# Performance work log

Measured on AMD Instinct MI355X. Metric: run time of the kernel, lower is better.

Reference implementation:

```python
import jax, jax.numpy as jnp
import numpy as np

L, B, S, D, H, FF = 6, 4, 1024, 256, 8, 128
DH = D // H
EPS = 1e-5


def _ln(x, w, b):
    m = x.mean(-1, keepdims=True)
    v = ((x - m) ** 2).mean(-1, keepdims=True)
    return (x - m) / jnp.sqrt(v + EPS) * w + b


def setup_inputs() -> dict:
    key = jax.random.key(0)
    ks = jax.random.split(key, 6)
    s = lambda k, shape: jax.random.normal(k, shape, jnp.float32) * 0.02
    return {
        "x": jax.random.normal(ks[0], (B, S, D), jnp.float32),
        "ln1_w": jnp.ones((L, D), jnp.float32),
        "ln1_b": jnp.zeros((L, D), jnp.float32),
        "wqkv": s(ks[1], (L, D, 3 * D)),   # qkv_linear, bias=False
        "wout": s(ks[2], (L, D, D)),       # out_linear, bias=False
        "ln2_w": jnp.ones((L, D), jnp.float32),
        "ln2_b": jnp.zeros((L, D), jnp.float32),
        "w1": s(ks[3], (L, D, 2 * FF)),    # Linear(d_model, 2*ff)
        "b1": jnp.zeros((L, 2 * FF), jnp.float32),
        "w2": s(ks[4], (L, FF, D)),        # Linear(ff, d_model)
        "b2": jnp.zeros((L, D), jnp.float32),
    }


def reference(x, ln1_w, ln1_b, wqkv, wout, ln2_w, ln2_b, w1, b1, w2, b2):
    attn_weights_list = []
    scale = 1.0 / jnp.sqrt(jnp.float32(DH))
    for i in range(L):
        # --- pre-norm multi-head attention ---
        xn = _ln(x, ln1_w[i], ln1_b[i])
        qkv = xn @ wqkv[i]                       # [B,S,3D]
        q, k, v = jnp.split(qkv, 3, axis=-1)
        rs = lambda t: t.reshape(B, S, H, DH).transpose(0, 2, 1, 3)  # b h s d
        q, k, v = rs(q), rs(k), rs(v)
        logits = jnp.einsum('bhid,bhjd->bhij', q, k) * scale
        aw = jax.nn.softmax(logits, axis=-1)     # [B,H,S,S] (dropout=0, eval)
        attn_weights_list.append(aw)
        o = jnp.einsum('bhij,bhjd->bhid', aw, v)
        o = o.transpose(0, 2, 1, 3).reshape(B, S, D) @ wout[i]
        x = x + o
        # --- pre-norm GEGLU FFN ---
        h = _ln(x, ln2_w[i], ln2_b[i]) @ w1[i] + b1[i]   # [B,S,2*FF]
        a, g = jnp.split(h, 2, axis=-1)
        x = x + (a * jax.nn.gelu(g, approximate=False)) @ w2[i] + b2[i]
    return x, jnp.stack(attn_weights_list)      # [B,S,D], [L,B,H,S,S]
```

## Files before the change

### kernel.cpp

```cpp
#include <hip/hip_runtime.h>
#include <hip/hip_bf16.h>

typedef __bf16 bf16x8 __attribute__((ext_vector_type(8)));
typedef __bf16 bf16x4 __attribute__((ext_vector_type(4)));
typedef float  f32x4  __attribute__((ext_vector_type(4)));

#define LAYERS 6
#define BATCH  4
#define SEQ    1024
#define DMODEL 256
#define NHEAD  8
#define DHEAD  32
#define FFDIM  128
#define ROWS   (BATCH*SEQ)
#define QKVN   (3*DMODEL)
#define QSCALE 0.2550348616f

static __device__ __forceinline__ bf16x8 ldg8(const __bf16* p) {
  return *reinterpret_cast<const bf16x8*>(p);
}
#define MFMA16(a, b, c) __builtin_amdgcn_mfma_f32_16x16x32_bf16((a), (b), (c), 0, 0, 0)

__global__ __launch_bounds__(256) void k_prepT(const float* __restrict__ in,
                                               __bf16* __restrict__ out,
                                               int R, int C) {
  __shared__ __bf16 T[64][72];
  int l = blockIdx.z, r0 = blockIdx.y * 64, c0 = blockIdx.x * 64;
  const float* src = in + ((size_t)l * R + r0) * C + c0;
  int tr = threadIdx.x >> 6, tc = threadIdx.x & 63;
  #pragma unroll 4
  for (int it = 0; it < 16; ++it) {
    int r = it * 4 + tr;
    T[r][tc] = (__bf16)src[(size_t)r * C + tc];
  }
  __syncthreads();
  __bf16* dst = out + ((size_t)l * C + c0) * R + r0;
  #pragma unroll 4
  for (int it = 0; it < 16; ++it) {
    int c = it * 4 + tr;
    dst[(size_t)c * R + tc] = T[tc][c];
  }
}

__global__ __launch_bounds__(64) void k_ln(const float* __restrict__ x,
                                           const float* __restrict__ w,
                                           const float* __restrict__ b,
                                           __bf16* __restrict__ out) {
  int row = blockIdx.x, l = threadIdx.x;
  const float* xr = x + (size_t)row * DMODEL;
  float v[4];
  #pragma unroll
  for (int j = 0; j < 4; ++j) v[j] = xr[l + 64 * j];
  float s = v[0] + v[1] + v[2] + v[3];
  #pragma unroll
  for (int off = 32; off >= 1; off >>= 1) s += __shfl_xor(s, off);
  float mean = s * (1.0f / DMODEL);
  float sq = 0.f;
  #pragma unroll
  for (int j = 0; j < 4; ++j) { v[j] -= mean; sq += v[j] * v[j]; }
  #pragma unroll
  for (int off = 32; off >= 1; off >>= 1) sq += __shfl_xor(sq, off);
  float rstd = rsqrtf(sq * (1.0f / DMODEL) + 1e-5f);
  __bf16* orow = out + (size_t)row * DMODEL;
  #pragma unroll
  for (int j = 0; j < 4; ++j) {
    int c = l + 64 * j;
    orow[c] = (__bf16)(v[j] * rstd * w[c] + b[c]);
  }
}

__global__ __launch_bounds__(256) void k_qkv(const __bf16* __restrict__ xn,
                                             const __bf16* __restrict__ Bt,
                                             __bf16* __restrict__ qb,
                                             __bf16* __restrict__ kt,
                                             __bf16* __restrict__ vt) {
  int w = threadIdx.x >> 6, l = threadIdx.x & 63, lr = l & 15, lg = l >> 4;
  int m0 = blockIdx.x * 64 + w * 16;
  int n0 = blockIdx.y * 64;
  f32x4 acc[4] = {};
  const __bf16* ap = xn + (size_t)(m0 + lr) * DMODEL + 8 * lg;
  const __bf16* bp = Bt + (size_t)(n0 + lr) * DMODEL + 8 * lg;
  for (int kc = 0; kc < DMODEL; kc += 32) {
    bf16x8 a = ldg8(ap + kc);
    #pragma unroll
    for (int t = 0; t < 4; ++t) {
      bf16x8 b = ldg8(bp + (size_t)t * 16 * DMODEL + kc);
      acc[t] = MFMA16(a, b, acc[t]);
    }
  }
  int row = m0 + lg * 4;
  if (n0 < DMODEL) {
    #pragma unroll
    for (int t = 0; t < 4; ++t) {
      int col = n0 + t * 16 + lr;
      #pragma unroll
      for (int r = 0; r < 4; ++r)
        qb[(size_t)(row + r) * DMODEL + col] = (__bf16)(acc[t][r] * QSCALE);
    }
  } else if (n0 < 2 * DMODEL) {
    int b_ = row >> 10, s = row & (SEQ - 1);
    #pragma unroll
    for (int t = 0; t < 4; ++t) {
      int hdh = n0 - DMODEL + t * 16 + lr;
      int h = hdh >> 5, dh = hdh & 31;
      size_t base = ((size_t)(b_ * NHEAD + h) * SEQ + s) * DHEAD + dh;
      #pragma unroll
      for (int r = 0; r < 4; ++r) kt[base + (size_t)r * DHEAD] = (__bf16)acc[t][r];
    }
  } else {
    int b_ = row >> 10, s = row & (SEQ - 1);
    #pragma unroll
    for (int t = 0; t < 4; ++t) {
      int hdh = n0 - 2 * DMODEL + t * 16 + lr;
      int h = hdh >> 5, dh = hdh & 31;
      bf16x4 v4;
      #pragma unroll
      for (int r = 0; r < 4; ++r) v4[r] = (__bf16)acc[t][r];
      *reinterpret_cast<bf16x4*>(vt + ((size_t)(b_ * NHEAD + h) * DHEAD + dh) * SEQ + s) = v4;
    }
  }
}

__global__ __launch_bounds__(512, 6) void k_attn(const __bf16* __restrict__ qb,
                                                 const __bf16* __restrict__ kt,
                                                 const __bf16* __restrict__ vt,
                                                 __bf16* __restrict__ ob,
                                                 float* __restrict__ aw) {
  __shared__ __bf16 P[8][2][16][40];
  __shared__ float  Ssum[8][16];
  __shared__ float  OS[8][16][34];
  int bid = blockIdx.x;
  int swz = (bid & 7) * 256 + (bid >> 3);
  int qblk = swz & 63, h = (swz >> 6) & 7, b = swz >> 9;
  int w = threadIdx.x >> 6, l = threadIdx.x & 63, lr = l & 15, lg = l >> 4;
  int q0 = qblk * 16;
  bf16x8 qf = ldg8(qb + ((size_t)(b * SEQ) + q0 + lr) * DMODEL + h * DHEAD + 8 * lg);
  const __bf16* ktb = kt + (size_t)(b * NHEAD + h) * SEQ * DHEAD + 8 * lg;
  const __bf16* vtb = vt + (size_t)(b * NHEAD + h) * DHEAD * SEQ;
  f32x4 z = {};
  int kbeg = w * 128;

  float s4[4] = {0.f, 0.f, 0.f, 0.f};
  #pragma unroll 4
  for (int t = 0; t < 8; ++t) {
    bf16x8 kf = ldg8(ktb + (size_t)(kbeg + t * 16 + lr) * DHEAD);
    f32x4 d = MFMA16(qf, kf, z);
    #pragma unroll
    for (int r = 0; r < 4; ++r) s4[r] += exp2f(d[r]);
  }
  #pragma unroll
  for (int off = 1; off < 16; off <<= 1) {
    #pragma unroll
    for (int r = 0; r < 4; ++r) s4[r] += __shfl_xor(s4[r], off);
  }
  if (lr == 0) {
    #pragma unroll
    for (int r = 0; r < 4; ++r) Ssum[w][lg * 4 + r] = s4[r];
  }
  __syncthreads();
  float rinv[4];
  #pragma unroll
  for (int r = 0; r < 4; ++r) {
    int row = lg * 4 + r;
    float s = Ssum[0][row] + Ssum[1][row] + Ssum[2][row] + Ssum[3][row]
            + Ssum[4][row] + Ssum[5][row] + Ssum[6][row] + Ssum[7][row];
    rinv[r] = 1.0f / s;
  }

  float* awb = aw + ((size_t)(b * NHEAD + h) * SEQ) * SEQ;
  float (*ST)[32] = reinterpret_cast<float(*)[32]>(&OS[w][0][0]);

#define QK_TILE(KC, BUF)                                                          \
  {                                                                               \
    _Pragma("unroll")                                                             \
    for (int half = 0; half < 2; ++half) {                                        \
      int k0 = (KC) + half * 16;                                                  \
      bf16x8 kf = ldg8(ktb + (size_t)(k0 + lr) * DHEAD);                          \
      f32x4 d = MFMA16(qf, kf, z);                                                \
      _Pragma("unroll")                                                           \
      for (int r = 0; r < 4; ++r) {                                               \
        float pn = exp2f(d[r]) * rinv[r];                                         \
        ST[lg * 4 + r][half * 16 + lr] = pn;                                      \
        P[w][BUF][lg * 4 + r][half * 16 + lr] = (__bf16)pn;                       \
      }                                                                           \
    }                                                                             \
  }

#define FLUSH(KC)                                                                 \
  {                                                                               \
    int frow = l >> 3, fcol = (l & 7) * 4;                                        \
    f32x4 v0 = *reinterpret_cast<const f32x4*>(&ST[frow][fcol]);                  \
    f32x4 v1 = *reinterpret_cast<const f32x4*>(&ST[frow + 8][fcol]);              \
    *reinterpret_cast<f32x4*>(&awb[(size_t)(q0 + frow) * SEQ + (KC) + fcol]) = v0;\
    *reinterpret_cast<f32x4*>(&awb[(size_t)(q0 + frow + 8) * SEQ + (KC) + fcol]) = v1;\
  }

  f32x4 accO[2] = {};
  QK_TILE(kbeg, 0)
  #pragma unroll
  for (int j = 1; j < 4; ++j) {
    int kc = kbeg + j * 32;
    bf16x8 pf  = *reinterpret_cast<const bf16x8*>(&P[w][(j - 1) & 1][lr][8 * lg]);
    bf16x8 vf0 = ldg8(vtb + (size_t)lr * SEQ + (kc - 32) + 8 * lg);
    bf16x8 vf1 = ldg8(vtb + (size_t)(16 + lr) * SEQ + (kc - 32) + 8 * lg);
    FLUSH(kc - 32)
    QK_TILE(kc, j & 1)
    accO[0] = MFMA16(pf, vf0, accO[0]);
    accO[1] = MFMA16(pf, vf1, accO[1]);
  }
  {
    bf16x8 pf  = *reinterpret_cast<const bf16x8*>(&P[w][1][lr][8 * lg]);
    bf16x8 vf0 = ldg8(vtb + (size_t)lr * SEQ + (kbeg + 96) + 8 * lg);
    bf16x8 vf1 = ldg8(vtb + (size_t)(16 + lr) * SEQ + (kbeg + 96) + 8 * lg);
    FLUSH(kbeg + 96)
    accO[0] = MFMA16(pf, vf0, accO[0]);
    accO[1] = MFMA16(pf, vf1, accO[1]);
  }
#undef QK_TILE
#undef FLUSH

  #pragma unroll
  for (int t = 0; t < 2; ++t)
    #pragma unroll
    for (int r = 0; r < 4; ++r) OS[w][lg * 4 + r][t * 16 + lr] = accO[t][r];
  __syncthreads();
  int row = threadIdx.x >> 5, col = threadIdx.x & 31;
  float o = 0.f;
  #pragma unroll
  for (int ww = 0; ww < 8; ++ww) o += OS[ww][row][col];
  ob[((size_t)(b * SEQ) + q0 + row) * DMODEL + h * DHEAD + col] = (__bf16)o;
}

template <int LAST>
__global__ __launch_bounds__(512) void k_pf(const __bf16* __restrict__ ob,
                                            const __bf16* __restrict__ woutT,
                                            const float* __restrict__ xres,
                                            const float* __restrict__ ln2w,
                                            const float* __restrict__ ln2b,
                                            const __bf16* __restrict__ w1t,
                                            const float* __restrict__ b1,
                                            const __bf16* __restrict__ w2t,
                                            const float* __restrict__ b2,
                                            float* __restrict__ x32out,
                                            const float* __restrict__ lnw_n,
                                            const float* __restrict__ lnb_n,
                                            const __bf16* __restrict__ wqkvT_n,
                                            __bf16* __restrict__ qb,
                                            __bf16* __restrict__ kt,
                                            __bf16* __restrict__ vt,
                                            float* __restrict__ xout) {
  __shared__ float  xs[16][268];
  __shared__ __bf16 XN[16][264];
  __shared__ __bf16 HT[16][136];
  int w = threadIdx.x >> 6, l = threadIdx.x & 63, lr = l & 15, lg = l >> 4;
  int m0 = blockIdx.x * 16;
  {
    int n0 = w * 32;
    f32x4 acc[2] = {};
    const __bf16* ap = ob + (size_t)(m0 + lr) * DMODEL + 8 * lg;
    const __bf16* bp = woutT + (size_t)(n0 + lr) * DMODEL + 8 * lg;
    for (int kc = 0; kc < DMODEL; kc += 32) {
      bf16x8 a = ldg8(ap + kc);
      #pragma unroll
      for (int t = 0; t < 2; ++t)
        acc[t] = MFMA16(a, ldg8(bp + (size_t)t * 16 * DMODEL + kc), acc[t]);
    }
    #pragma unroll
    for (int t = 0; t < 2; ++t) {
      int col = n0 + t * 16 + lr;
      #pragma unroll
      for (int r = 0; r < 4; ++r) {
        int row = lg * 4 + r;
        xs[row][col] = acc[t][r] + xres[(size_t)(m0 + row) * DMODEL + col];
      }
    }
  }
  __syncthreads();
  #pragma unroll
  for (int rr = 0; rr < 2; ++rr) {
    int row = w * 2 + rr;
    f32x4 v = *reinterpret_cast<const f32x4*>(&xs[row][4 * l]);
    float s = v[0] + v[1] + v[2] + v[3];
    #pragma unroll
    for (int off = 32; off >= 1; off >>= 1) s += __shfl_xor(s, off);
    float mean = s * (1.0f / DMODEL);
    float sq = 0.f;
    f32x4 c;
    #pragma unroll
    for (int j = 0; j < 4; ++j) { c[j] = v[j] - mean; sq += c[j] * c[j]; }
    #pragma unroll
    for (int off = 32; off >= 1; off >>= 1) sq += __shfl_xor(sq, off);
    float rstd = rsqrtf(sq * (1.0f / DMODEL) + 1e-5f);
    f32x4 lwv = *reinterpret_cast<const f32x4*>(&ln2w[4 * l]);
    f32x4 lbv = *reinterpret_cast<const f32x4*>(&ln2b[4 * l]);
    bf16x4 o4;
    #pragma unroll
    for (int j = 0; j < 4; ++j) o4[j] = (__bf16)(c[j] * rstd * lwv[j] + lbv[j]);
    *reinterpret_cast<bf16x4*>(&XN[row][4 * l]) = o4;
  }
  __syncthreads();
  {
    f32x4 acc1[2] = {};
    const __bf16* bpa = w1t + (size_t)(w * 16 + lr) * DMODEL + 8 * lg;
    const __bf16* bpg = w1t + (size_t)(128 + w * 16 + lr) * DMODEL + 8 * lg;
    for (int kc = 0; kc < DMODEL; kc += 32) {
      bf16x8 a = *reinterpret_cast<const bf16x8*>(&XN[lr][kc + 8 * lg]);
      acc1[0] = MFMA16(a, ldg8(bpa + kc), acc1[0]);
      acc1[1] = MFMA16(a, ldg8(bpg + kc), acc1[1]);
    }
    int fc = w * 16 + lr;
    #pragma unroll
    for (int r = 0; r < 4; ++r) {
      float a1 = acc1[0][r] + b1[fc];
      float g  = acc1[1][r] + b1[fc + 128];
      float ge = 0.5f * g * (1.0f + erff(g * 0.70710678118654752f));
      HT[lg * 4 + r][fc] = (__bf16)(a1 * ge);
    }
  }
  __syncthreads();
  {
    int n0 = w * 32;
    f32x4 acc2[2] = {};
    const __bf16* bp = w2t + (size_t)(n0 + lr) * FFDIM + 8 * lg;
    for (int kc = 0; kc < FFDIM; kc += 32) {
      bf16x8 a2 = *reinterpret_cast<const bf16x8*>(&HT[lr][kc + 8 * lg]);
      #pragma unroll
      for (int t = 0; t < 2; ++t)
        acc2[t] = MFMA16(a2, ldg8(bp + (size_t)t * 16 * FFDIM + kc), acc2[t]);
    }
    #pragma unroll
    for (int t = 0; t < 2; ++t) {
      int col = n0 + t * 16 + lr;
      #pragma unroll
      for (int r = 0; r < 4; ++r) {
        int row = lg * 4 + r;
        xs[row][col] = acc2[t][r] + b2[col] + xs[row][col];
      }
    }
  }
  __syncthreads();
  #pragma unroll
  for (int rr = 0; rr < 2; ++rr) {
    int row = w * 2 + rr;
    f32x4 v = *reinterpret_cast<const f32x4*>(&xs[row][4 * l]);
    if (LAST) {
      *reinterpret_cast<f32x4*>(&xout[(size_t)(m0 + row) * DMODEL + 4 * l]) = v;
    } else {
      float s = v[0] + v[1] + v[2] + v[3];
      #pragma unroll
      for (int off = 32; off >= 1; off >>= 1) s += __shfl_xor(s, off);
      float mean = s * (1.0f / DMODEL);
      float sq = 0.f;
      f32x4 c;
      #pragma unroll
      for (int j = 0; j < 4; ++j) { c[j] = v[j] - mean; sq += c[j] * c[j]; }
      #pragma unroll
      for (int off = 32; off >= 1; off >>= 1) sq += __shfl_xor(sq, off);
      float rstd = rsqrtf(sq * (1.0f / DMODEL) + 1e-5f);
      *reinterpret_cast<f32x4*>(&x32out[(size_t)(m0 + row) * DMODEL + 4 * l]) = v;
      f32x4 lwv = *reinterpret_cast<const f32x4*>(&lnw_n[4 * l]);
      f32x4 lbv = *reinterpret_cast<const f32x4*>(&lnb_n[4 * l]);
      bf16x4 o4;
      #pragma unroll
      for (int j = 0; j < 4; ++j) o4[j] = (__bf16)(c[j] * rstd * lwv[j] + lbv[j]);
      *reinterpret_cast<bf16x4*>(&XN[row][4 * l]) = o4;
    }
  }
  if (!LAST) {
    __syncthreads();
    f32x4 acc[6] = {};
    {
      const __bf16* bp = wqkvT_n + (size_t)(w * 96 + lr) * DMODEL + 8 * lg;
      for (int kc = 0; kc < DMODEL; kc += 32) {
        bf16x8 a = *reinterpret_cast<const bf16x8*>(&XN[lr][kc + 8 * lg]);
        #pragma unroll
        for (int t = 0; t < 6; ++t)
          acc[t] = MFMA16(a, ldg8(bp + (size_t)t * 16 * DMODEL + kc), acc[t]);
      }
    }
    int row = m0 + lg * 4;
    int b_ = row >> 10, s = row & (SEQ - 1);
    #pragma unroll
    for (int t = 0; t < 6; ++t) {
      int col = w * 96 + t * 16 + lr;
      if (col < DMODEL) {
        #pragma unroll
        for (int r = 0; r < 4; ++r)
          qb[(size_t)(row + r) * DMODEL + col] = (__bf16)(acc[t][r] * QSCALE);
      } else if (col < 2 * DMODEL) {
        int hdh = col - DMODEL;
        int h = hdh >> 5, dh = hdh & 31;
        size_t base = ((size_t)(b_ * NHEAD + h) * SEQ + s) * DHEAD + dh;
        #pragma unroll
        for (int r = 0; r < 4; ++r) kt[base + (size_t)r * DHEAD] = (__bf16)acc[t][r];
      } else {
        int hdh = col - 2 * DMODEL;
        int h = hdh >> 5, dh = hdh & 31;
        bf16x4 v4;
        #pragma unroll
        for (int r = 0; r < 4; ++r) v4[r] = (__bf16)acc[t][r];
        *reinterpret_cast<bf16x4*>(vt + ((size_t)(b_ * NHEAD + h) * DHEAD + dh) * SEQ + s) = v4;
      }
    }
  }
}

static inline size_t align256(size_t x) { return (x + 255) & ~(size_t)255; }

extern "C" void kernel_launch(void* const* d_in, const int* in_sizes, int n_in,
                              void* d_out, int out_size, void* d_ws, size_t ws_size,
                              hipStream_t stream) {
  const float* x_in = (const float*)d_in[0];
  const float* ln1w = (const float*)d_in[1];
  const float* ln1b = (const float*)d_in[2];
  const float* wqkv = (const float*)d_in[3];
  const float* wout = (const float*)d_in[4];
  const float* ln2w = (const float*)d_in[5];
  const float* ln2b = (const float*)d_in[6];
  const float* w1   = (const float*)d_in[7];
  const float* b1   = (const float*)d_in[8];
  const float* w2   = (const float*)d_in[9];
  const float* b2   = (const float*)d_in[10];
  float* out = (float*)d_out;

  char* p = (char*)d_ws;
  float*  x32   = (float*)p;  p += align256((size_t)ROWS * DMODEL * 4);
  __bf16* xn    = (__bf16*)p; p += align256((size_t)ROWS * DMODEL * 2);
  __bf16* qb    = (__bf16*)p; p += align256((size_t)ROWS * DMODEL * 2);
  __bf16* kt    = (__bf16*)p; p += align256((size_t)ROWS * DMODEL * 2);
  __bf16* vt    = (__bf16*)p; p += align256((size_t)ROWS * DMODEL * 2);
  __bf16* ob    = (__bf16*)p; p += align256((size_t)ROWS * DMODEL * 2);
  __bf16* wqkvT = (__bf16*)p; p += align256((size_t)LAYERS * DMODEL * QKVN * 2);
  __bf16* woutT = (__bf16*)p; p += align256((size_t)LAYERS * DMODEL * DMODEL * 2);
  __bf16* w1T   = (__bf16*)p; p += align256((size_t)LAYERS * DMODEL * 2 * FFDIM * 2);
  __bf16* w2T   = (__bf16*)p; p += align256((size_t)LAYERS * FFDIM * DMODEL * 2);

  k_prepT<<<dim3(QKVN / 64, DMODEL / 64, LAYERS), 256, 0, stream>>>(wqkv, wqkvT, DMODEL, QKVN);
  k_prepT<<<dim3(DMODEL / 64, DMODEL / 64, LAYERS), 256, 0, stream>>>(wout, woutT, DMODEL, DMODEL);
  k_prepT<<<dim3(2 * FFDIM / 64, DMODEL / 64, LAYERS), 256, 0, stream>>>(w1, w1T, DMODEL, 2 * FFDIM);
  k_prepT<<<dim3(DMODEL / 64, FFDIM / 64, LAYERS), 256, 0, stream>>>(w2, w2T, FFDIM, DMODEL);
  k_ln<<<ROWS, 64, 0, stream>>>(x_in, ln1w, ln1b, xn);
  k_qkv<<<dim3(ROWS / 64, QKVN / 64), 256, 0, stream>>>(xn, wqkvT, qb, kt, vt);

  const size_t AW_LAYER = (size_t)BATCH * NHEAD * SEQ * SEQ;
  for (int i = 0; i < LAYERS; ++i) {
    float* aw_l = out + (size_t)ROWS * DMODEL + (size_t)i * AW_LAYER;
    k_attn<<<SEQ / 16 * NHEAD * BATCH, 512, 0, stream>>>(qb, kt, vt, ob, aw_l);
    const float* xres = (i == 0) ? x_in : x32;
    if (i < LAYERS - 1) {
      k_pf<0><<<ROWS / 16, 512, 0, stream>>>(
          ob, woutT + (size_t)i * DMODEL * DMODEL, xres,
          ln2w + i * DMODEL, ln2b + i * DMODEL,
          w1T + (size_t)i * DMODEL * 2 * FFDIM, b1 + i * 2 * FFDIM,
          w2T + (size_t)i * FFDIM * DMODEL, b2 + i * DMODEL,
          x32, ln1w + (i + 1) * DMODEL, ln1b + (i + 1) * DMODEL,
          wqkvT + (size_t)(i + 1) * DMODEL * QKVN, qb, kt, vt, nullptr);
    } else {
      k_pf<1><<<ROWS / 16, 512, 0, stream>>>(
          ob, woutT + (size_t)i * DMODEL * DMODEL, xres,
          ln2w + i * DMODEL, ln2b + i * DMODEL,
          w1T + (size_t)i * DMODEL * 2 * FFDIM, b1 + i * 2 * FFDIM,
          w2T + (size_t)i * FFDIM * DMODEL, b2 + i * DMODEL,
          x32, nullptr, nullptr, nullptr, nullptr, nullptr, nullptr, out);
    }
  }
}
```

Measured before the change: 444.7 us.

## Move attention-weight writes into fused post-attention kernel with double-buffered QKV

The attention kernel now does a single pass: it accumulates unnormalized softmax sums alongside the PV product, normalizes the output at the end, and stores per-row reciprocal sums. The big fp32 attention-weight writes move into extra blocks of the fused out-proj/FFN/next-QKV kernel, which recompute QK^T, scale by the stored reciprocals, and write with nontemporal stores. QKV buffers are double-buffered so the next layer's projections do not overwrite data those blocks still read. This removes the separate sum pre-pass and overlaps the memory-bound weight stores with FFN compute, at the cost of recomputing the QK^T product and extra workspace.

New measurement: 460.5 us. +3.6%, slower.

```diff
diff --git a/kernel.cpp b/kernel.cpp
--- a/kernel.cpp
+++ b/kernel.cpp
@@ -15,6 +15,8 @@
 #define ROWS   (BATCH*SEQ)
 #define QKVN   (3*DMODEL)
 #define QSCALE 0.2550348616f
+#define PFBLKS (ROWS/16)
+#define AWBLKS (SEQ/16*NHEAD*BATCH)
 
 static __device__ __forceinline__ bf16x8 ldg8(const __bf16* p) {
   return *reinterpret_cast<const bf16x8*>(p);
@@ -125,7 +127,7 @@
                                                  const __bf16* __restrict__ kt,
                                                  const __bf16* __restrict__ vt,
                                                  __bf16* __restrict__ ob,
-                                                 float* __restrict__ aw) {
+                                                 float* __restrict__ rb) {
   __shared__ __bf16 P[8][2][16][40];
   __shared__ float  Ssum[8][16];
   __shared__ float  OS[8][16][34];
@@ -141,34 +143,6 @@
   int kbeg = w * 128;
 
   float s4[4] = {0.f, 0.f, 0.f, 0.f};
-  #pragma unroll 4
-  for (int t = 0; t < 8; ++t) {
-    bf16x8 kf = ldg8(ktb + (size_t)(kbeg + t * 16 + lr) * DHEAD);
-    f32x4 d = MFMA16(qf, kf, z);
-    #pragma unroll
-    for (int r = 0; r < 4; ++r) s4[r] += exp2f(d[r]);
-  }
-  #pragma unroll
-  for (int off = 1; off < 16; off <<= 1) {
-    #pragma unroll
-    for (int r = 0; r < 4; ++r) s4[r] += __shfl_xor(s4[r], off);
-  }
-  if (lr == 0) {
-    #pragma unroll
-    for (int r = 0; r < 4; ++r) Ssum[w][lg * 4 + r] = s4[r];
-  }
-  __syncthreads();
-  float rinv[4];
-  #pragma unroll
-  for (int r = 0; r < 4; ++r) {
-    int row = lg * 4 + r;
-    float s = Ssum[0][row] + Ssum[1][row] + Ssum[2][row] + Ssum[3][row]
-            + Ssum[4][row] + Ssum[5][row] + Ssum[6][row] + Ssum[7][row];
-    rinv[r] = 1.0f / s;
-  }
-
-  float* awb = aw + ((size_t)(b * NHEAD + h) * SEQ) * SEQ;
-  float (*ST)[32] = reinterpret_cast<float(*)[32]>(&OS[w][0][0]);
 
 #define QK_TILE(KC, BUF)                                                          \
   {                                                                               \
@@ -179,20 +153,11 @@
       f32x4 d = MFMA16(qf, kf, z);                                                \
       _Pragma("unroll")                                                           \
       for (int r = 0; r < 4; ++r) {                                               \
-        float pn = exp2f(d[r]) * rinv[r];                                         \
-        ST[lg * 4 + r][half * 16 + lr] = pn;                                      \
-        P[w][BUF][lg * 4 + r][half * 16 + lr] = (__bf16)pn;                       \
+        float pv = exp2f(d[r]);                                                   \
+        s4[r] += pv;                                                              \
+        P[w][BUF][lg * 4 + r][half * 16 + lr] = (__bf16)pv;                       \
       }                                                                           \
     }                                                                             \
-  }
-
-#define FLUSH(KC)                                                                 \
-  {                                                                               \
-    int frow = l >> 3, fcol = (l & 7) * 4;                                        \
-    f32x4 v0 = *reinterpret_cast<const f32x4*>(&ST[frow][fcol]);                  \
-    f32x4 v1 = *reinterpret_cast<const f32x4*>(&ST[frow + 8][fcol]);              \
-    *reinterpret_cast<f32x4*>(&awb[(size_t)(q0 + frow) * SEQ + (KC) + fcol]) = v0;\
-    *reinterpret_cast<f32x4*>(&awb[(size_t)(q0 + frow + 8) * SEQ + (KC) + fcol]) = v1;\
   }
 
   f32x4 accO[2] = {};
@@ -203,7 +168,6 @@
     bf16x8 pf  = *reinterpret_cast<const bf16x8*>(&P[w][(j - 1) & 1][lr][8 * lg]);
     bf16x8 vf0 = ldg8(vtb + (size_t)lr * SEQ + (kc - 32) + 8 * lg);
     bf16x8 vf1 = ldg8(vtb + (size_t)(16 + lr) * SEQ + (kc - 32) + 8 * lg);
-    FLUSH(kc - 32)
     QK_TILE(kc, j & 1)
     accO[0] = MFMA16(pf, vf0, accO[0]);
     accO[1] = MFMA16(pf, vf1, accO[1]);
@@ -212,17 +176,40 @@
     bf16x8 pf  = *reinterpret_cast<const bf16x8*>(&P[w][1][lr][8 * lg]);
     bf16x8 vf0 = ldg8(vtb + (size_t)lr * SEQ + (kbeg + 96) + 8 * lg);
     bf16x8 vf1 = ldg8(vtb + (size_t)(16 + lr) * SEQ + (kbeg + 96) + 8 * lg);
-    FLUSH(kbeg + 96)
     accO[0] = MFMA16(pf, vf0, accO[0]);
     accO[1] = MFMA16(pf, vf1, accO[1]);
   }
 #undef QK_TILE
-#undef FLUSH
+
+  #pragma unroll
+  for (int off = 1; off < 16; off <<= 1) {
+    #pragma unroll
+    for (int r = 0; r < 4; ++r) s4[r] += __shfl_xor(s4[r], off);
+  }
+  if (lr == 0) {
+    #pragma unroll
+    for (int r = 0; r < 4; ++r) Ssum[w][lg * 4 + r] = s4[r];
+  }
+  __syncthreads();
+  float rinv[4];
+  #pragma unroll
+  for (int r = 0; r < 4; ++r) {
+    int row = lg * 4 + r;
+    float s = Ssum[0][row] + Ssum[1][row] + Ssum[2][row] + Ssum[3][row]
+            + Ssum[4][row] + Ssum[5][row] + Ssum[6][row] + Ssum[7][row];
+    rinv[r] = 1.0f / s;
+  }
+  if (w == 0 && l < 16) {
+    float s = 0.f;
+    #pragma unroll
+    for (int ww = 0; ww < 8; ++ww) s += Ssum[ww][l];
+    rb[((size_t)(b * SEQ) + q0 + l) * NHEAD + h] = 1.0f / s;
+  }
 
   #pragma unroll
   for (int t = 0; t < 2; ++t)
     #pragma unroll
-    for (int r = 0; r < 4; ++r) OS[w][lg * 4 + r][t * 16 + lr] = accO[t][r];
+    for (int r = 0; r < 4; ++r) OS[w][lg * 4 + r][t * 16 + lr] = accO[t][r] * rinv[r];
   __syncthreads();
   int row = threadIdx.x >> 5, col = threadIdx.x & 31;
   float o = 0.f;
@@ -232,27 +219,69 @@
 }
 
 template <int LAST>
-__global__ __launch_bounds__(512) void k_pf(const __bf16* __restrict__ ob,
-                                            const __bf16* __restrict__ woutT,
-                                            const float* __restrict__ xres,
-                                            const float* __restrict__ ln2w,
-                                            const float* __restrict__ ln2b,
-                                            const __bf16* __restrict__ w1t,
-                                            const float* __restrict__ b1,
-                                            const __bf16* __restrict__ w2t,
-                                            const float* __restrict__ b2,
-                                            float* __restrict__ x32out,
-                                            const float* __restrict__ lnw_n,
-                                            const float* __restrict__ lnb_n,
-                                            const __bf16* __restrict__ wqkvT_n,
-                                            __bf16* __restrict__ qb,
-                                            __bf16* __restrict__ kt,
-                                            __bf16* __restrict__ vt,
-                                            float* __restrict__ xout) {
-  __shared__ float  xs[16][268];
-  __shared__ __bf16 XN[16][264];
-  __shared__ __bf16 HT[16][136];
+__global__ __launch_bounds__(512) void k_pfaw(const __bf16* __restrict__ ob,
+                                              const __bf16* __restrict__ qbr,
+                                              const __bf16* __restrict__ ktr,
+                                              const float* __restrict__ rb,
+                                              float* __restrict__ aw,
+                                              const __bf16* __restrict__ woutT,
+                                              const float* __restrict__ xres,
+                                              const float* __restrict__ ln2w,
+                                              const float* __restrict__ ln2b,
+                                              const __bf16* __restrict__ w1t,
+                                              const float* __restrict__ b1,
+                                              const __bf16* __restrict__ w2t,
+                                              const float* __restrict__ b2,
+                                              float* __restrict__ x32out,
+                                              const float* __restrict__ lnw_n,
+                                              const float* __restrict__ lnb_n,
+                                              const __bf16* __restrict__ wqkvT_n,
+                                              __bf16* __restrict__ qb_n,
+                                              __bf16* __restrict__ kt_n,
+                                              __bf16* __restrict__ vt_n,
+                                              float* __restrict__ xout) {
+  __shared__ char smem[17152 + 8448 + 4352];
   int w = threadIdx.x >> 6, l = threadIdx.x & 63, lr = l & 15, lg = l >> 4;
+
+  if (blockIdx.x >= PFBLKS) {
+    float (*ST)[16][32] = reinterpret_cast<float(*)[16][32]>(smem);
+    int bid = blockIdx.x - PFBLKS;
+    int swz = (bid & 7) * 256 + (bid >> 3);
+    int qblk = swz & 63, h = (swz >> 6) & 7, b = swz >> 9;
+    int q0 = qblk * 16;
+    bf16x8 qf = ldg8(qbr + ((size_t)(b * SEQ) + q0 + lr) * DMODEL + h * DHEAD + 8 * lg);
+    const __bf16* ktb = ktr + (size_t)(b * NHEAD + h) * SEQ * DHEAD + 8 * lg;
+    float rv[4];
+    #pragma unroll
+    for (int r = 0; r < 4; ++r)
+      rv[r] = rb[((size_t)(b * SEQ) + q0 + lg * 4 + r) * NHEAD + h];
+    float* awb = aw + ((size_t)(b * NHEAD + h) * SEQ) * SEQ;
+    f32x4 z = {};
+    int kbeg = w * 128;
+    #pragma unroll
+    for (int t0 = 0; t0 < 8; ++t0) {
+      bf16x8 kf = ldg8(ktb + (size_t)(kbeg + t0 * 16 + lr) * DHEAD);
+      f32x4 d = MFMA16(qf, kf, z);
+      #pragma unroll
+      for (int r = 0; r < 4; ++r)
+        ST[w][lg * 4 + r][(t0 & 1) * 16 + lr] = exp2f(d[r]) * rv[r];
+      if (t0 & 1) {
+        int frow = l >> 3, fcol = (l & 7) * 4;
+        int kc = kbeg + (t0 - 1) * 16;
+        f32x4 v0 = *reinterpret_cast<const f32x4*>(&ST[w][frow][fcol]);
+        f32x4 v1 = *reinterpret_cast<const f32x4*>(&ST[w][frow + 8][fcol]);
+        __builtin_nontemporal_store(v0, reinterpret_cast<f32x4*>(
+            &awb[(size_t)(q0 + frow) * SEQ + kc + fcol]));
+        __builtin_nontemporal_store(v1, reinterpret_cast<f32x4*>(
+            &awb[(size_t)(q0 + frow + 8) * SEQ + kc + fcol]));
+      }
+    }
+    return;
+  }
+
+  float  (*xs)[268] = reinterpret_cast<float(*)[268]>(smem);
+  __bf16 (*XN)[264] = reinterpret_cast<__bf16(*)[264]>(smem + 17152);
+  __bf16 (*HT)[136] = reinterpret_cast<__bf16(*)[136]>(smem + 17152 + 8448);
   int m0 = blockIdx.x * 16;
   {
     int n0 = w * 32;
@@ -386,20 +415,20 @@
       if (col < DMODEL) {
         #pragma unroll
         for (int r = 0; r < 4; ++r)
-          qb[(size_t)(row + r) * DMODEL + col] = (__bf16)(acc[t][r] * QSCALE);
+          qb_n[(size_t)(row + r) * DMODEL + col] = (__bf16)(acc[t][r] * QSCALE);
       } else if (col < 2 * DMODEL) {
         int hdh = col - DMODEL;
         int h = hdh >> 5, dh = hdh & 31;
         size_t base = ((size_t)(b_ * NHEAD + h) * SEQ + s) * DHEAD + dh;
         #pragma unroll
-        for (int r = 0; r < 4; ++r) kt[base + (size_t)r * DHEAD] = (__bf16)acc[t][r];
+        for (int r = 0; r < 4; ++r) kt_n[base + (size_t)r * DHEAD] = (__bf16)acc[t][r];
       } else {
         int hdh = col - 2 * DMODEL;
         int h = hdh >> 5, dh = hdh & 31;
         bf16x4 v4;
         #pragma unroll
         for (int r = 0; r < 4; ++r) v4[r] = (__bf16)acc[t][r];
-        *reinterpret_cast<bf16x4*>(vt + ((size_t)(b_ * NHEAD + h) * DHEAD + dh) * SEQ + s) = v4;
+        *reinterpret_cast<bf16x4*>(vt_n + ((size_t)(b_ * NHEAD + h) * DHEAD + dh) * SEQ + s) = v4;
       }
     }
   }
@@ -426,10 +455,14 @@
   char* p = (char*)d_ws;
   float*  x32   = (float*)p;  p += align256((size_t)ROWS * DMODEL * 4);
   __bf16* xn    = (__bf16*)p; p += align256((size_t)ROWS * DMODEL * 2);
-  __bf16* qb    = (__bf16*)p; p += align256((size_t)ROWS * DMODEL * 2);
-  __bf16* kt    = (__bf16*)p; p += align256((size_t)ROWS * DMODEL * 2);
-  __bf16* vt    = (__bf16*)p; p += align256((size_t)ROWS * DMODEL * 2);
+  __bf16* qbA   = (__bf16*)p; p += align256((size_t)ROWS * DMODEL * 2);
+  __bf16* ktA   = (__bf16*)p; p += align256((size_t)ROWS * DMODEL * 2);
+  __bf16* vtA   = (__bf16*)p; p += align256((size_t)ROWS * DMODEL * 2);
+  __bf16* qbB   = (__bf16*)p; p += align256((size_t)ROWS * DMODEL * 2);
+  __bf16* ktB   = (__bf16*)p; p += align256((size_t)ROWS * DMODEL * 2);
+  __bf16* vtB   = (__bf16*)p; p += align256((size_t)ROWS * DMODEL * 2);
   __bf16* ob    = (__bf16*)p; p += align256((size_t)ROWS * DMODEL * 2);
+  float*  rb    = (float*)p;  p += align256((size_t)ROWS * NHEAD * 4);
   __bf16* wqkvT = (__bf16*)p; p += align256((size_t)LAYERS * DMODEL * QKVN * 2);
   __bf16* woutT = (__bf16*)p; p += align256((size_t)LAYERS * DMODEL * DMODEL * 2);
   __bf16* w1T   = (__bf16*)p; p += align256((size_t)LAYERS * DMODEL * 2 * FFDIM * 2);
@@ -440,24 +473,32 @@
   k_prepT<<<dim3(2 * FFDIM / 64, DMODEL / 64, LAYERS), 256, 0, stream>>>(w1, w1T, DMODEL, 2 * FFDIM);
   k_prepT<<<dim3(DMODEL / 64, FFDIM / 64, LAYERS), 256, 0, stream>>>(w2, w2T, FFDIM, DMODEL);
   k_ln<<<ROWS, 64, 0, stream>>>(x_in, ln1w, ln1b, xn);
-  k_qkv<<<dim3(ROWS / 64, QKVN / 64), 256, 0, stream>>>(xn, wqkvT, qb, kt, vt);
+  k_qkv<<<dim3(ROWS / 64, QKVN / 64), 256, 0, stream>>>(xn, wqkvT, qbA, ktA, vtA);
 
   const size_t AW_LAYER = (size_t)BATCH * NHEAD * SEQ * SEQ;
   for (int i = 0; i < LAYERS; ++i) {
     float* aw_l = out + (size_t)ROWS * DMODEL + (size_t)i * AW_LAYER;
-    k_attn<<<SEQ / 16 * NHEAD * BATCH, 512, 0, stream>>>(qb, kt, vt, ob, aw_l);
     const float* xres = (i == 0) ? x_in : x32;
+    __bf16* qb_c = (i & 1) ? qbB : qbA;
+    __bf16* kt_c = (i & 1) ? ktB : ktA;
+    __bf16* vt_c = (i & 1) ? vtB : vtA;
+    __bf16* qb_n = (i & 1) ? qbA : qbB;
+    __bf16* kt_n = (i & 1) ? ktA : ktB;
+    __bf16* vt_n = (i & 1) ? vtA : vtB;
+    k_attn<<<AWBLKS, 512, 0, stream>>>(qb_c, kt_c, vt_c, ob, rb);
     if (i < LAYERS - 1) {
-      k_pf<0><<<ROWS / 16, 512, 0, stream>>>(
-          ob, woutT + (size_t)i * DMODEL * DMODEL, xres,
+      k_pfaw<0><<<PFBLKS + AWBLKS, 512, 0, stream>>>(
+          ob, qb_c, kt_c, rb, aw_l,
+          woutT + (size_t)i * DMODEL * DMODEL, xres,
           ln2w + i * DMODEL, ln2b + i * DMODEL,
           w1T + (size_t)i * DMODEL * 2 * FFDIM, b1 + i * 2 * FFDIM,
           w2T + (size_t)i * FFDIM * DMODEL, b2 + i * DMODEL,
           x32, ln1w + (i + 1) * DMODEL, ln1b + (i + 1) * DMODEL,
-          wqkvT + (size_t)(i + 1) * DMODEL * QKVN, qb, kt, vt, nullptr);
+          wqkvT + (size_t)(i + 1) * DMODEL * QKVN, qb_n, kt_n, vt_n, nullptr);
     } else {
-      k_pf<1><<<ROWS / 16, 512, 0, stream>>>(
-          ob, woutT + (size_t)i * DMODEL * DMODEL, xres,
+      k_pfaw<1><<<PFBLKS + AWBLKS, 512, 0, stream>>>(
+          ob, qb_c, kt_c, rb, aw_l,
+          woutT + (size_t)i * DMODEL * DMODEL, xres,
           ln2w + i * DMODEL, ln2b + i * DMODEL,
           w1T + (size_t)i * DMODEL * 2 * FFDIM, b1 + i * 2 * FFDIM,
           w2T + (size_t)i * FFDIM * DMODEL, b2 + i * DMODEL,
```
